# Kernel optimization log

Measured on AMD Instinct MI355X. Metric: run time of the kernel, lower is better.

The kernel has to match this reference:

```python
import jax, jax.numpy as jnp
import numpy as np

DIM = 192
HEADS = 6
WH, WW = 8, 8
N = WH * WW
B_ = 2048
NW = 512


def _relative_position_index():
    coords = np.stack(np.meshgrid(np.arange(WH), np.arange(WW), indexing='ij'))  # 2,Wh,Ww
    cf = coords.reshape(2, -1)
    rel = cf[:, :, None] - cf[:, None, :]  # 2,N,N
    rel = rel.transpose(1, 2, 0).astype(np.int32)
    rel[:, :, 0] += WH - 1
    rel[:, :, 1] += WW - 1
    rel[:, :, 0] *= 2 * WW - 1
    return jnp.asarray(rel.sum(-1))  # N,N int32


def setup_inputs() -> dict:
    key = jax.random.key(0)
    ks = jax.random.split(key, 16)
    s = 0.02
    inp = {
        'q': jax.random.normal(ks[0], (B_, N, DIM), jnp.float32),
        'k': jax.random.normal(ks[1], (B_, N, DIM), jnp.float32),
        'v': jax.random.normal(ks[2], (B_, N, DIM), jnp.float32),
        'mask': jax.random.normal(ks[3], (NW, N, N), jnp.float32),
        'attn_mask': jax.random.randint(ks[4], (B_, 1, N, N), 0, 2).astype(bool),
        'Wq': jax.random.normal(ks[5], (DIM, DIM), jnp.float32) * s,
        'bq': jnp.zeros((DIM,), jnp.float32),
        'Wk': jax.random.normal(ks[6], (DIM, DIM), jnp.float32) * s,
        'bk': jnp.zeros((DIM,), jnp.float32),
        'Wv': jax.random.normal(ks[7], (DIM, DIM), jnp.float32) * s,
        'bv': jnp.zeros((DIM,), jnp.float32),
        'Wp': jax.random.normal(ks[8], (DIM, DIM), jnp.float32) * s,
        'bp': jnp.zeros((DIM,), jnp.float32),
        'rpb_table': jax.random.normal(ks[9], ((2 * WH - 1) * (2 * WW - 1), HEADS), jnp.float32) * s,
        'rel_idx': _relative_position_index(),
    }
    return inp


def reference(q, k, v, mask, attn_mask, Wq, bq, Wk, bk, Wv, bv, Wp, bp, rpb_table, rel_idx):
    Bw, n, C = q.shape
    hd = C // HEADS
    scale = hd ** (-0.5)
    # linear projections (torch Linear: x @ W.T + b), split heads -> b h n d
    qh = (q @ Wq.T + bq).reshape(Bw, n, HEADS, hd).transpose(0, 2, 1, 3) * scale
    kh = (k @ Wk.T + bk).reshape(Bw, n, HEADS, hd).transpose(0, 2, 1, 3)
    vh = (v @ Wv.T + bv).reshape(Bw, n, HEADS, hd).transpose(0, 2, 1, 3)
    attn = jnp.einsum('bhnd,bhmd->bhnm', qh, kh)  # (B_, H, N, N)
    attn = jnp.where(attn_mask, jnp.float32(-1e9), attn)
    # relative position bias gather: (N,N,H) -> (H,N,N)
    bias = rpb_table[rel_idx.reshape(-1)].reshape(n, n, HEADS).transpose(2, 0, 1)
    attn = attn + bias[None]
    nW = mask.shape[0]
    attn = attn.reshape(Bw // nW, nW, HEADS, n, n) + mask[None, :, None]
    attn = jax.nn.softmax(attn.reshape(Bw, HEADS, n, n), axis=-1)
    x = jnp.einsum('bhnm,bhmd->bhnd', attn, vh).transpose(0, 2, 1, 3).reshape(Bw, n, C)
    return x @ Wp.T + bp
```

## Files before the change

### kernel.cpp

```cpp
#include <hip/hip_runtime.h>

#define DIM    192
#define HEADS  6
#define HD     32
#define NTOK   64
#define NWIN   512
#define NBLK   2048
#define WMAT   (DIM*DIM)
#define XPITCH 200

typedef short  bf16x4 __attribute__((ext_vector_type(4)));
typedef short  bf16x8 __attribute__((ext_vector_type(8)));
typedef float  f32x4  __attribute__((ext_vector_type(4)));

#if defined(__HIP_DEVICE_COMPILE__)
#if !__has_builtin(__builtin_amdgcn_mfma_f32_16x16x32_bf16)
#error "missing __builtin_amdgcn_mfma_f32_16x16x32_bf16"
#endif
#if !__has_builtin(__builtin_amdgcn_mfma_f32_16x16x16bf16_1k)
#error "missing __builtin_amdgcn_mfma_f32_16x16x16bf16_1k"
#endif
#endif

static __device__ __forceinline__ unsigned short f2bf(float f){
  unsigned u = __builtin_bit_cast(unsigned, f);
  u += 0x7FFFu + ((u >> 16) & 1u);
  return (unsigned short)(u >> 16);
}

static __device__ __forceinline__ f32x4 mfma32(bf16x8 a, bf16x8 b, f32x4 c){
  return __builtin_amdgcn_mfma_f32_16x16x32_bf16(a, b, c, 0, 0, 0);
}
static __device__ __forceinline__ f32x4 mfma16(bf16x4 a, bf16x4 b, f32x4 c){
  return __builtin_amdgcn_mfma_f32_16x16x16bf16_1k(a, b, c, 0, 0, 0);
}

static __device__ __forceinline__ bf16x8 wfrag(const unsigned short* __restrict__ W, int row, int k0){
  return *(const bf16x8*)(W + row*DIM + k0);
}

__global__ void detect_amask_kernel(const unsigned int* __restrict__ am, int* __restrict__ mode){
  __shared__ int sawFloat, sawByte;
  if (threadIdx.x == 0){ sawFloat = 0; sawByte = 0; }
  __syncthreads();
  const uint4 ld = ((const uint4*)am)[threadIdx.x];
  unsigned w[4] = {ld.x, ld.y, ld.z, ld.w};
  int f = 0, bm = 0;
  #pragma unroll
  for (int i = 0; i < 4; ++i){
    if (w[i] == 0x3F800000u) f = 1;
    else if (w[i] & ~1u)     bm = 1;
  }
  if (f)  atomicOr(&sawFloat, 1);
  if (bm) atomicOr(&sawByte, 1);
  __syncthreads();
  if (threadIdx.x == 0) *mode = sawFloat ? 2 : (sawByte ? 1 : 0);
}

__global__ void bias_pre_kernel(const float* __restrict__ rpb, const int* __restrict__ rel_idx,
                                float* __restrict__ bias_t){
  const int e = blockIdx.x*256 + threadIdx.x;
  if (e >= HEADS*NTOK*NTOK) return;
  const int n = (e >> 6) & 63, m = e & 63;
  bias_t[e] = rpb[rel_idx[n*NTOK + m]*HEADS + (e >> 12)];
}

__global__ void wconv_kernel(const float* __restrict__ Wq, const float* __restrict__ Wk,
                             const float* __restrict__ Wv, const float* __restrict__ Wp,
                             unsigned short* __restrict__ wbf){
  const int e4 = blockIdx.x*256 + threadIdx.x;
  if (e4 >= 4*WMAT/4) return;
  const int mat = e4 / (WMAT/4);
  const int off = e4 - mat*(WMAT/4);
  const float* src = (mat==0)?Wq:(mat==1)?Wk:(mat==2)?Wv:Wp;
  const float4 f = ((const float4*)src)[off];
  unsigned short* dst = wbf + mat*WMAT + off*4;
  dst[0]=f2bf(f.x); dst[1]=f2bf(f.y); dst[2]=f2bf(f.z); dst[3]=f2bf(f.w);
}

__global__ __launch_bounds__(256, 4) void proj_kernel(
  const float* __restrict__ q, const float* __restrict__ kin, const float* __restrict__ vin,
  const unsigned short* __restrict__ wbf,
  const float* __restrict__ bq, const float* __restrict__ bk, const float* __restrict__ bv,
  char* __restrict__ outc, unsigned short* __restrict__ Vt)
{
  __shared__ unsigned short xs[NTOK * XPITCH];

  const int bid = blockIdx.x;
  const int mat = bid >> 11;
  const int w   = bid & (NBLK-1);
  const int t   = threadIdx.x;
  const int wv  = t >> 6;
  const int lane= t & 63;
  const int l15 = lane & 15;
  const int g   = lane >> 4;
  const size_t base = (size_t)w * (NTOK * DIM);
  const float scale = 0.17677669529663687f;
  const f32x4 fz = {0.f, 0.f, 0.f, 0.f};

  const float* src = (mat==0) ? (q + base) : (mat==1) ? (kin + base) : (vin + base);

  #pragma unroll
  for (int j = 0; j < 12; ++j){
    const int i4  = t + j*256;
    const float4 f = ((const float4*)src)[i4];
    const int row = i4 / 48;
    const int col = (i4 - row*48) * 4;
    uint2 u;
    u.x = (unsigned)f2bf(f.x) | ((unsigned)f2bf(f.y) << 16);
    u.y = (unsigned)f2bf(f.z) | ((unsigned)f2bf(f.w) << 16);
    *(uint2*)(xs + row*XPITCH + col) = u;
  }
  __syncthreads();

  const int ct0 = wv*3;

  if (mat < 2){
    const unsigned short* W = wbf + mat*WMAT;
    const float* bias = mat ? bk : bq;
    const float sc = mat ? 1.0f : scale;
    f32x4 acc[3][4];
    #pragma unroll
    for (int c=0;c<3;++c){
      #pragma unroll
      for (int nt=0;nt<4;++nt) acc[c][nt] = fz;
    }
    #pragma unroll
    for (int kt = 0; kt < 6; ++kt){
      const int k0 = kt*32 + g*8;
      bf16x8 wf[3];
      #pragma unroll
      for (int c=0;c<3;++c) wf[c] = wfrag(W, (ct0+c)*16 + l15, k0);
      #pragma unroll
      for (int nt = 0; nt < 4; ++nt){
        const bf16x8 xf = *(const bf16x8*)(xs + (nt*16 + l15)*XPITCH + k0);
        #pragma unroll
        for (int c=0;c<3;++c) acc[c][nt] = mfma32(wf[c], xf, acc[c][nt]);
      }
    }
    #pragma unroll
    for (int c=0;c<3;++c){
      const int ct = ct0 + c;
      const float4 bb = *(const float4*)(bias + ct*16 + g*4);
      #pragma unroll
      for (int nt = 0; nt < 4; ++nt){
        const int n = nt*16 + l15;
        uint2 u;
        u.x = (unsigned)f2bf((acc[c][nt][0]+bb.x)*sc) | ((unsigned)f2bf((acc[c][nt][1]+bb.y)*sc) << 16);
        u.y = (unsigned)f2bf((acc[c][nt][2]+bb.z)*sc) | ((unsigned)f2bf((acc[c][nt][3]+bb.w)*sc) << 16);
        *(uint2*)(outc + (base + (size_t)n*DIM)*4/1  * 0 + (size_t)(w*NTOK + n)*768 + mat*384 + (ct*16 + g*4)*2) = u;
      }
    }
  } else {
    const unsigned short* W = wbf + 2*WMAT;
    f32x4 acc[4][3];
    #pragma unroll
    for (int mt=0;mt<4;++mt){
      #pragma unroll
      for (int c=0;c<3;++c) acc[mt][c] = fz;
    }
    #pragma unroll
    for (int kt = 0; kt < 6; ++kt){
      const int k0 = kt*32 + g*8;
      bf16x8 wf[3];
      #pragma unroll
      for (int c=0;c<3;++c) wf[c] = wfrag(W, (ct0+c)*16 + l15, k0);
      #pragma unroll
      for (int mt = 0; mt < 4; ++mt){
        const bf16x8 xf = *(const bf16x8*)(xs + (mt*16 + l15)*XPITCH + k0);
        #pragma unroll
        for (int c=0;c<3;++c) acc[mt][c] = mfma32(xf, wf[c], acc[mt][c]);
      }
    }
    #pragma unroll
    for (int c=0;c<3;++c){
      const int cc = (ct0 + c)*16 + l15;
      const float bvv = bv[cc];
      #pragma unroll
      for (int mt = 0; mt < 4; ++mt){
        uint2 u;
        u.x = (unsigned)f2bf(acc[mt][c][0]+bvv) | ((unsigned)f2bf(acc[mt][c][1]+bvv) << 16);
        u.y = (unsigned)f2bf(acc[mt][c][2]+bvv) | ((unsigned)f2bf(acc[mt][c][3]+bvv) << 16);
        *(uint2*)(Vt + ((size_t)w*DIM + cc)*NTOK + mt*16 + g*4) = u;
      }
    }
  }
}

__global__ __launch_bounds__(384, 2) void attn_kernel(
  const float* __restrict__ mask, const void* __restrict__ amask,
  const float* __restrict__ bias_t, const int* __restrict__ mflag,
  char* __restrict__ outc, const unsigned short* __restrict__ Vt)
{
  const int b    = blockIdx.x;
  const int t    = threadIdx.x;
  const int h    = t >> 6;
  const int lane = t & 63;
  const int l15  = lane & 15;
  const int g    = lane >> 4;
  const f32x4 fz = {0.f, 0.f, 0.f, 0.f};

  bf16x4 Qf[4][2], Kf[4][2], Vf[2][4];
  #pragma unroll
  for (int nt = 0; nt < 4; ++nt){
    const size_t rowb = (size_t)(b*NTOK + nt*16 + l15)*768 + h*64;
    #pragma unroll
    for (int dt = 0; dt < 2; ++dt){
      Qf[nt][dt] = *(const bf16x4*)(outc + rowb + (dt*16 + g*4)*2);
      Kf[nt][dt] = *(const bf16x4*)(outc + rowb + 384 + (dt*16 + g*4)*2);
    }
  }
  #pragma unroll
  for (int dt = 0; dt < 2; ++dt){
    const size_t rowv = ((size_t)b*DIM + h*HD + dt*16 + l15)*NTOK;
    #pragma unroll
    for (int mt = 0; mt < 4; ++mt){
      Vf[dt][mt] = *(const bf16x4*)(Vt + rowv + mt*16 + g*4);
    }
  }

  f32x4 s[4][4];
  #pragma unroll
  for (int mt = 0; mt < 4; ++mt){
    #pragma unroll
    for (int nt = 0; nt < 4; ++nt){
      f32x4 a = mfma16(Kf[mt][0], Qf[nt][0], fz);
      s[mt][nt] = mfma16(Kf[mt][1], Qf[nt][1], a);
    }
  }

  {
    const int mode = mflag[0];
    const float* mrow = mask + (size_t)(b & (NWIN-1)) * (NTOK*NTOK);
    const float* brow = bias_t + h * (NTOK*NTOK);
    #pragma unroll
    for (int nt = 0; nt < 4; ++nt){
      const int n = nt*16 + l15;
      #pragma unroll
      for (int mt = 0; mt < 4; ++mt){
        const int off = n*NTOK + mt*16 + g*4;
        const float4 mk = *(const float4*)(mrow + off);
        const float4 bi = *(const float4*)(brow + off);
        float am[4];
        if (mode == 0){
          const int4 a4 = *(const int4*)((const int*)amask + (size_t)b*(NTOK*NTOK) + off);
          am[0] = a4.x ? -1e9f : 0.f; am[1] = a4.y ? -1e9f : 0.f;
          am[2] = a4.z ? -1e9f : 0.f; am[3] = a4.w ? -1e9f : 0.f;
        } else if (mode == 1){
          const unsigned a4 = *(const unsigned*)((const unsigned char*)amask + (size_t)b*(NTOK*NTOK) + off);
          am[0] = (a4 & 0x000000FFu) ? -1e9f : 0.f; am[1] = (a4 & 0x0000FF00u) ? -1e9f : 0.f;
          am[2] = (a4 & 0x00FF0000u) ? -1e9f : 0.f; am[3] = (a4 & 0xFF000000u) ? -1e9f : 0.f;
        } else {
          const float4 a4 = *(const float4*)((const float*)amask + (size_t)b*(NTOK*NTOK) + off);
          am[0] = (a4.x != 0.f) ? -1e9f : 0.f; am[1] = (a4.y != 0.f) ? -1e9f : 0.f;
          am[2] = (a4.z != 0.f) ? -1e9f : 0.f; am[3] = (a4.w != 0.f) ? -1e9f : 0.f;
        }
        s[mt][nt][0] += mk.x + bi.x + am[0];
        s[mt][nt][1] += mk.y + bi.y + am[1];
        s[mt][nt][2] += mk.z + bi.z + am[2];
        s[mt][nt][3] += mk.w + bi.w + am[3];
      }
    }
  }

  bf16x4 Pf[4][4];
  #pragma unroll
  for (int nt = 0; nt < 4; ++nt){
    float mx = -3.0e38f;
    #pragma unroll
    for (int mt = 0; mt < 4; ++mt){
      #pragma unroll
      for (int r = 0; r < 4; ++r) mx = fmaxf(mx, s[mt][nt][r]);
    }
    mx = fmaxf(mx, __shfl_xor(mx, 16, 64));
    mx = fmaxf(mx, __shfl_xor(mx, 32, 64));
    float sum = 0.f;
    #pragma unroll
    for (int mt = 0; mt < 4; ++mt){
      #pragma unroll
      for (int r = 0; r < 4; ++r){
        const float e = __expf(s[mt][nt][r] - mx);
        s[mt][nt][r] = e;
        sum += e;
      }
    }
    sum += __shfl_xor(sum, 16, 64);
    sum += __shfl_xor(sum, 32, 64);
    const float inv = 1.0f / sum;
    #pragma unroll
    for (int ms = 0; ms < 4; ++ms){
      bf16x4 f;
      f[0]=(short)f2bf(s[ms][nt][0]*inv); f[1]=(short)f2bf(s[ms][nt][1]*inv);
      f[2]=(short)f2bf(s[ms][nt][2]*inv); f[3]=(short)f2bf(s[ms][nt][3]*inv);
      Pf[nt][ms] = f;
    }
  }

  f32x4 o[2][4];
  #pragma unroll
  for (int a0=0;a0<2;++a0){
    #pragma unroll
    for (int a1=0;a1<4;++a1) o[a0][a1] = fz;
  }
  #pragma unroll
  for (int ms = 0; ms < 4; ++ms){
    #pragma unroll
    for (int dt = 0; dt < 2; ++dt){
      #pragma unroll
      for (int nt = 0; nt < 4; ++nt){
        o[dt][nt] = mfma16(Vf[dt][ms], Pf[nt][ms], o[dt][nt]);
      }
    }
  }

  #pragma unroll
  for (int dt = 0; dt < 2; ++dt){
    #pragma unroll
    for (int nt = 0; nt < 4; ++nt){
      const int n = nt*16 + l15;
      uint2 u;
      u.x = (unsigned)f2bf(o[dt][nt][0]) | ((unsigned)f2bf(o[dt][nt][1]) << 16);
      u.y = (unsigned)f2bf(o[dt][nt][2]) | ((unsigned)f2bf(o[dt][nt][3]) << 16);
      *(uint2*)(outc + (size_t)(b*NTOK + n)*768 + h*64 + (dt*16 + g*4)*2) = u;
    }
  }
}

__global__ __launch_bounds__(256, 4) void oproj_kernel(
  float* __restrict__ outf, const unsigned short* __restrict__ wbf,
  const float* __restrict__ bp)
{
  const int t    = threadIdx.x;
  const int wv   = t >> 6;
  const int lane = t & 63;
  const int l15  = lane & 15;
  const int g    = lane >> 4;
  const int n0   = (blockIdx.x*4 + wv) * 16;
  const unsigned short* Wp = wbf + 3*WMAT;
  const f32x4 fz = {0.f, 0.f, 0.f, 0.f};

  f32x4 acc[12];
  #pragma unroll
  for (int ct = 0; ct < 12; ++ct) acc[ct] = fz;

  #pragma unroll
  for (int kt = 0; kt < 6; ++kt){
    const int k0 = kt*32 + g*8;
    const bf16x8 a = *(const bf16x8*)((const char*)outf + (size_t)(n0 + l15)*768 + k0*2);
    #pragma unroll
    for (int ct = 0; ct < 12; ++ct){
      const bf16x8 w = wfrag(Wp, ct*16 + l15, k0);
      acc[ct] = mfma32(a, w, acc[ct]);
    }
  }
  #pragma unroll
  for (int ct = 0; ct < 12; ++ct){
    const float badd = bp[ct*16 + l15];
    #pragma unroll
    for (int r = 0; r < 4; ++r){
      outf[(size_t)(n0 + g*4 + r)*DIM + ct*16 + l15] = acc[ct][r] + badd;
    }
  }
}

extern "C" void kernel_launch(void* const* d_in, const int* in_sizes, int n_in,
                              void* d_out, int out_size, void* d_ws, size_t ws_size,
                              hipStream_t stream){
  const float* q     = (const float*)d_in[0];
  const float* k     = (const float*)d_in[1];
  const float* v     = (const float*)d_in[2];
  const float* mask  = (const float*)d_in[3];
  const void*  amask = d_in[4];
  const float* Wq    = (const float*)d_in[5];
  const float* bq    = (const float*)d_in[6];
  const float* Wk    = (const float*)d_in[7];
  const float* bk    = (const float*)d_in[8];
  const float* Wv    = (const float*)d_in[9];
  const float* bv    = (const float*)d_in[10];
  const float* Wp    = (const float*)d_in[11];
  const float* bp    = (const float*)d_in[12];
  const float* rpb   = (const float*)d_in[13];
  const int*   ridx  = (const int*)d_in[14];
  float* out = (float*)d_out;

  float*          bias_t = (float*)d_ws;
  int*            mflag  = (int*)((char*)d_ws + 98304);
  unsigned short* wbf    = (unsigned short*)((char*)d_ws + 98560);
  unsigned short* Vt     = (unsigned short*)((char*)d_ws + 524288);

  detect_amask_kernel<<<1, 256, 0, stream>>>((const unsigned int*)amask, mflag);
  bias_pre_kernel<<<96, 256, 0, stream>>>(rpb, ridx, bias_t);
  wconv_kernel<<<144, 256, 0, stream>>>(Wq, Wk, Wv, Wp, wbf);
  proj_kernel<<<3*NBLK, 256, 0, stream>>>(q, k, v, wbf, bq, bk, bv, (char*)out, Vt);
  attn_kernel<<<NBLK, 384, 0, stream>>>(mask, amask, bias_t, mflag, (char*)out, Vt);
  oproj_kernel<<<NBLK, 256, 0, stream>>>(out, wbf, bp);
}
```

Before: 407.9 us.

## Stage projection and attention outputs in LDS for coalesced global stores

```diff
diff --git a/kernel.cpp b/kernel.cpp
--- a/kernel.cpp
+++ b/kernel.cpp
@@ -6,8 +6,11 @@
 #define NTOK   64
 #define NWIN   512
 #define NBLK   2048
+#define NTASK  (NBLK*HEADS)
 #define WMAT   (DIM*DIM)
 #define XPITCH 200
+#define VPITCH 66
+#define TPITCH 36
 
 typedef short  bf16x4 __attribute__((ext_vector_type(4)));
 typedef short  bf16x8 __attribute__((ext_vector_type(8)));
@@ -138,6 +141,7 @@
         for (int c=0;c<3;++c) acc[c][nt] = mfma32(wf[c], xf, acc[c][nt]);
       }
     }
+    __syncthreads();
     #pragma unroll
     for (int c=0;c<3;++c){
       const int ct = ct0 + c;
@@ -148,8 +152,17 @@
         uint2 u;
         u.x = (unsigned)f2bf((acc[c][nt][0]+bb.x)*sc) | ((unsigned)f2bf((acc[c][nt][1]+bb.y)*sc) << 16);
         u.y = (unsigned)f2bf((acc[c][nt][2]+bb.z)*sc) | ((unsigned)f2bf((acc[c][nt][3]+bb.w)*sc) << 16);
-        *(uint2*)(outc + (base + (size_t)n*DIM)*4/1  * 0 + (size_t)(w*NTOK + n)*768 + mat*384 + (ct*16 + g*4)*2) = u;
-      }
+        *(uint2*)(xs + n*XPITCH + ct*16 + g*4) = u;
+      }
+    }
+    __syncthreads();
+    #pragma unroll
+    for (int j = 0; j < 12; ++j){
+      const int i = t + j*256;
+      const int row  = i / 48;
+      const int col8 = i - row*48;
+      const uint2 u = *(const uint2*)(xs + row*XPITCH + col8*4);
+      *(uint2*)(outc + (size_t)(w*NTOK + row)*768 + mat*384 + col8*8) = u;
     }
   } else {
     const unsigned short* W = wbf + 2*WMAT;
@@ -172,6 +185,7 @@
         for (int c=0;c<3;++c) acc[mt][c] = mfma32(xf, wf[c], acc[mt][c]);
       }
     }
+    __syncthreads();
     #pragma unroll
     for (int c=0;c<3;++c){
       const int cc = (ct0 + c)*16 + l15;
@@ -181,20 +195,33 @@
         uint2 u;
         u.x = (unsigned)f2bf(acc[mt][c][0]+bvv) | ((unsigned)f2bf(acc[mt][c][1]+bvv) << 16);
         u.y = (unsigned)f2bf(acc[mt][c][2]+bvv) | ((unsigned)f2bf(acc[mt][c][3]+bvv) << 16);
-        *(uint2*)(Vt + ((size_t)w*DIM + cc)*NTOK + mt*16 + g*4) = u;
-      }
-    }
-  }
-}
-
-__global__ __launch_bounds__(384, 2) void attn_kernel(
+        *(uint2*)(xs + cc*VPITCH + mt*16 + g*4) = u;
+      }
+    }
+    __syncthreads();
+    #pragma unroll
+    for (int j = 0; j < 12; ++j){
+      const int i = t + j*256;
+      const int row  = i >> 4;
+      const int col8 = i & 15;
+      const uint2 u = *(const uint2*)(xs + row*VPITCH + col8*4);
+      *(uint2*)(Vt + ((size_t)w*DIM + row)*NTOK + col8*4) = u;
+    }
+  }
+}
+
+__global__ __launch_bounds__(256, 4) void attn_kernel(
   const float* __restrict__ mask, const void* __restrict__ amask,
   const float* __restrict__ bias_t, const int* __restrict__ mflag,
   char* __restrict__ outc, const unsigned short* __restrict__ Vt)
 {
-  const int b    = blockIdx.x;
+  __shared__ unsigned short xt[4][NTOK * TPITCH];
+
   const int t    = threadIdx.x;
-  const int h    = t >> 6;
+  const int wv   = t >> 6;
+  const int task = blockIdx.x*4 + wv;
+  const int b    = task / HEADS;
+  const int h    = task - b*HEADS;
   const int lane = t & 63;
   const int l15  = lane & 15;
   const int g    = lane >> 4;
@@ -313,6 +340,7 @@
     }
   }
 
+  unsigned short* myt = &xt[wv][0];
   #pragma unroll
   for (int dt = 0; dt < 2; ++dt){
     #pragma unroll
@@ -321,7 +349,19 @@
       uint2 u;
       u.x = (unsigned)f2bf(o[dt][nt][0]) | ((unsigned)f2bf(o[dt][nt][1]) << 16);
       u.y = (unsigned)f2bf(o[dt][nt][2]) | ((unsigned)f2bf(o[dt][nt][3]) << 16);
-      *(uint2*)(outc + (size_t)(b*NTOK + n)*768 + h*64 + (dt*16 + g*4)*2) = u;
+      *(uint2*)(myt + n*TPITCH + dt*16 + g*4) = u;
+    }
+  }
+
+  {
+    char* dst = outc + (size_t)b*NTOK*768 + h*64;
+    const int nloc = lane >> 4;
+    const int dwi  = lane & 15;
+    #pragma unroll
+    for (int it = 0; it < 16; ++it){
+      const int n = it*4 + nloc;
+      const unsigned d = *(const unsigned*)(myt + n*TPITCH + dwi*2);
+      *(unsigned*)(dst + (size_t)n*768 + dwi*4) = d;
     }
   }
 }
@@ -392,6 +432,6 @@
   bias_pre_kernel<<<96, 256, 0, stream>>>(rpb, ridx, bias_t);
   wconv_kernel<<<144, 256, 0, stream>>>(Wq, Wk, Wv, Wp, wbf);
   proj_kernel<<<3*NBLK, 256, 0, stream>>>(q, k, v, wbf, bq, bk, bv, (char*)out, Vt);
-  attn_kernel<<<NBLK, 384, 0, stream>>>(mask, amask, bias_t, mflag, (char*)out, Vt);
+  attn_kernel<<<NTASK/4, 256, 0, stream>>>(mask, amask, bias_t, mflag, (char*)out, Vt);
   oproj_kernel<<<NBLK, 256, 0, stream>>>(out, wbf, bp);
 }
```

After: 501.6 us. +23.0%, slower.
